# Optimization experiments

Measured on AMD Instinct MI355X. Metric: run time of the kernel, lower is better.

## Reference

```python
import jax, jax.numpy as jnp
import numpy as np

QMAX = 127.0  # symmetric int8
EPS = 1e-8

def _ste_round(v):
    # straight-through estimator round
    return v + jax.lax.stop_gradient(jnp.round(v) - v)

def fake_quant_act(x):
    # dynamic per-token symmetric 8-bit fake quant (last dim is features)
    scale = jnp.maximum(jnp.max(jnp.abs(x), axis=-1, keepdims=True) / QMAX, EPS)
    q = jnp.clip(_ste_round(x / scale), -QMAX, QMAX)
    return q * scale

def fake_quant_weight(w):
    # per-output-channel symmetric 8-bit fake quant; w: [out, in]
    scale = jnp.maximum(jnp.max(jnp.abs(w), axis=-1, keepdims=True) / QMAX, EPS)
    q = jnp.clip(_ste_round(w / scale), -QMAX, QMAX)
    return q * scale

def quant_linear(x, w):
    # fake-quant both operands, then dense matmul: [B,S,in] x [out,in] -> [B,S,out]
    return jnp.einsum('bsi,oi->bso', fake_quant_act(x), fake_quant_weight(w))

def setup_inputs() -> dict:
    key = jax.random.key(0)
    k1, k2, k3, k4 = jax.random.split(key, 4)
    B, S, H, I = 4, 2048, 2048, 6144
    return {
        'x': jax.random.normal(k1, (B, S, H), dtype=jnp.float32),
        'w_gate': jax.random.normal(k2, (I, H), dtype=jnp.float32) * 0.02,
        'w_up': jax.random.normal(k3, (I, H), dtype=jnp.float32) * 0.02,
        'w_down': jax.random.normal(k4, (H, I), dtype=jnp.float32) * 0.02,
    }

def reference(x, w_gate, w_up, w_down):
    gate = jax.nn.silu(quant_linear(x, w_gate))   # [B,S,I]
    up = quant_linear(x, w_up)                    # [B,S,I]
    return quant_linear(gate * up, w_down)        # [B,S,H]
```

## Files before the change

kernel.cpp:

```cpp
#include <hip/hip_runtime.h>
#include <hip/hip_bf16.h>
#include <math.h>

typedef __attribute__((ext_vector_type(4))) int intx4;

__device__ __forceinline__ void gload_lds16(const void* g, void* l) {
  __builtin_amdgcn_global_load_lds((__attribute__((address_space(1))) void*)g,
                                   (__attribute__((address_space(3))) void*)l,
                                   16, 0, 0);
}

__device__ __forceinline__ int pack4_i8(float a, float b, float c, float d) {
  return ((int)a & 255) | (((int)b & 255) << 8) | (((int)c & 255) << 16) | (((int)d & 255) << 24);
}

template<int NITER>
__global__ void quant_rows_i8_kernel(const float* __restrict__ src,
                                     signed char* __restrict__ dst,
                                     float* __restrict__ scales,
                                     int C) {
  const int row = blockIdx.x;
  const int t = threadIdx.x;
  const float4* s4 = (const float4*)(src + (size_t)row * C);
  float4 v[NITER];
  float amax = 0.0f;
#pragma unroll
  for (int i = 0; i < NITER; ++i) {
    v[i] = s4[t + (i << 8)];
    amax = fmaxf(amax, fmaxf(fmaxf(fabsf(v[i].x), fabsf(v[i].y)),
                             fmaxf(fabsf(v[i].z), fabsf(v[i].w))));
  }
#pragma unroll
  for (int off = 32; off > 0; off >>= 1)
    amax = fmaxf(amax, __shfl_xor(amax, off));
  __shared__ float red[4];
  if ((t & 63) == 0) red[t >> 6] = amax;
  __syncthreads();
  if (t == 0) {
    float m = fmaxf(fmaxf(red[0], red[1]), fmaxf(red[2], red[3]));
    float s = fmaxf(m * (1.0f / 127.0f), 1e-8f);
    red[0] = s;
    scales[row] = s;
  }
  __syncthreads();
  const float scale = red[0];
  int* o4 = (int*)(dst + (size_t)row * C);
#pragma unroll
  for (int i = 0; i < NITER; ++i) {
    const float q0 = fminf(fmaxf(rintf(v[i].x / scale), -127.0f), 127.0f);
    const float q1 = fminf(fmaxf(rintf(v[i].y / scale), -127.0f), 127.0f);
    const float q2 = fminf(fmaxf(rintf(v[i].z / scale), -127.0f), 127.0f);
    const float q3 = fminf(fmaxf(rintf(v[i].w / scale), -127.0f), 127.0f);
    o4[t + (i << 8)] = pack4_i8(q0, q1, q2, q3);
  }
}

template<bool DUAL>
__global__ __launch_bounds__(256, 2)
void gemm_i8_kernel(const signed char* __restrict__ A,
                    const signed char* __restrict__ B0,
                    const signed char* __restrict__ B1,
                    const float* __restrict__ sA,
                    const float* __restrict__ sB0,
                    const float* __restrict__ sB1,
                    float* __restrict__ out,
                    int N, int K) {
  extern __shared__ __align__(16) char smem[];
  char* const As  = smem;
  char* const Bs0 = smem + 16384;
  char* const Bs1 = smem + 32768;

  const int nTn = N >> 7;
  const int nwg = gridDim.x;
  const int bid = blockIdx.x;
  const int cpx = nwg >> 3;
  const int swz = (bid & 7) * cpx + (bid >> 3);
  const int tm = swz / nTn, tn = swz - tm * nTn;
  const int m0 = tm << 7, n0 = tn << 7;

  const int t = threadIdx.x;
  const int lane = t & 63;
  const int wid = t >> 6;
  const int wr = wid >> 1, wc = wid & 1;

  const intx4 zero = {0, 0, 0, 0};
  intx4 acc0[4][4];
  intx4 acc1[4][4];
#pragma unroll
  for (int i = 0; i < 4; ++i)
#pragma unroll
    for (int j = 0; j < 4; ++j) {
      acc0[i][j] = zero;
      if (DUAL) acc1[i][j] = zero;
    }

  for (int k0 = 0; k0 < K; k0 += 128) {
#pragma unroll
    for (int rr = 0; rr < 4; ++rr) {
      const int chunk = (rr << 8) + t;
      const int r = chunk >> 3;
      const int c8 = (chunk & 7) ^ (r & 7);
      gload_lds16(A + (size_t)(m0 + r) * K + (k0 + (c8 << 4)), As + (chunk << 4));
    }
#pragma unroll
    for (int rr = 0; rr < 4; ++rr) {
      const int chunk = (rr << 8) + t;
      const int r = chunk >> 3;
      const int c8 = (chunk & 7) ^ (r & 7);
      const size_t goff = (size_t)(n0 + r) * K + (k0 + (c8 << 4));
      gload_lds16(B0 + goff, Bs0 + (chunk << 4));
      if (DUAL) gload_lds16(B1 + goff, Bs1 + (chunk << 4));
    }
    __syncthreads();

#pragma unroll
    for (int ks = 0; ks < 2; ++ks) {
      intx4 af[4], bf0[4], bf1[4];
#pragma unroll
      for (int i = 0; i < 4; ++i) {
        const int r = (wr << 6) + (i << 4) + (lane & 15);
        const int c8 = (ks << 2) + (lane >> 4);
        af[i] = *(const intx4*)(As + r * 128 + ((c8 ^ (r & 7)) << 4));
      }
#pragma unroll
      for (int j = 0; j < 4; ++j) {
        const int r = (wc << 6) + (j << 4) + (lane & 15);
        const int c8 = (ks << 2) + (lane >> 4);
        const int off = r * 128 + ((c8 ^ (r & 7)) << 4);
        bf0[j] = *(const intx4*)(Bs0 + off);
        if (DUAL) bf1[j] = *(const intx4*)(Bs1 + off);
      }
#pragma unroll
      for (int i = 0; i < 4; ++i)
#pragma unroll
        for (int j = 0; j < 4; ++j) {
          acc0[i][j] = __builtin_amdgcn_mfma_i32_16x16x64_i8(af[i], bf0[j], acc0[i][j], 0, 0, 0);
          if (DUAL)
            acc1[i][j] = __builtin_amdgcn_mfma_i32_16x16x64_i8(af[i], bf1[j], acc1[i][j], 0, 0, 0);
        }
    }
    __syncthreads();
  }

  float sb0c[4], sb1c[4];
#pragma unroll
  for (int j = 0; j < 4; ++j) {
    const int col = n0 + (wc << 6) + (j << 4) + (lane & 15);
    sb0c[j] = sB0[col];
    if (DUAL) sb1c[j] = sB1[col];
  }
#pragma unroll
  for (int i = 0; i < 4; ++i) {
#pragma unroll
    for (int q = 0; q < 4; ++q) {
      const int row = m0 + (wr << 6) + (i << 4) + ((lane >> 4) << 2) + q;
      const float sa = sA[row];
      float* op = out + (size_t)row * N + n0 + (wc << 6) + (lane & 15);
#pragma unroll
      for (int j = 0; j < 4; ++j) {
        const float g = (float)acc0[i][j][q] * sa * sb0c[j];
        if (DUAL) {
          const float u = (float)acc1[i][j][q] * sa * sb1c[j];
          op[j << 4] = g / (1.0f + expf(-g)) * u;
        } else {
          op[j << 4] = g;
        }
      }
    }
  }
}

extern "C" void kernel_launch(void* const* d_in, const int* in_sizes, int n_in,
                              void* d_out, int out_size, void* d_ws, size_t ws_size,
                              hipStream_t stream) {
  const float* x  = (const float*)d_in[0];
  const float* wg = (const float*)d_in[1];
  const float* wu = (const float*)d_in[2];
  const float* wd = (const float*)d_in[3];
  float* out = (float*)d_out;

  const int M = 8192;
  const int H = 2048;
  const int I = 6144;

  char* ws = (char*)d_ws;
  signed char* xq  = (signed char*)(ws);
  signed char* wgq = (signed char*)(ws + 16777216);
  signed char* wuq = (signed char*)(ws + 29360128);
  signed char* wdq = (signed char*)(ws + 41943040);
  float* sx  = (float*)(ws + 54525952);
  float* swg = (float*)(ws + 54558720);
  float* swu = (float*)(ws + 54583296);
  float* swd = (float*)(ws + 54607872);
  float* sh  = (float*)(ws + 54616064);
  const size_t chunk_base = 54648832;

  size_t avail = (ws_size > chunk_base) ? (ws_size - chunk_base) : 0;
  long long c = (long long)(avail / ((size_t)I * 5));
  int CHUNK = (int)((c / 128) * 128);
  if (CHUNK > M) CHUNK = M;
  if (CHUNK < 128) CHUNK = 128;
  float* h = (float*)(ws + chunk_base);
  signed char* hq = (signed char*)(ws + chunk_base + (size_t)CHUNK * I * 4);

  quant_rows_i8_kernel<2><<<M, 256, 0, stream>>>(x,  xq,  sx,  H);
  quant_rows_i8_kernel<2><<<I, 256, 0, stream>>>(wg, wgq, swg, H);
  quant_rows_i8_kernel<2><<<I, 256, 0, stream>>>(wu, wuq, swu, H);
  quant_rows_i8_kernel<6><<<H, 256, 0, stream>>>(wd, wdq, swd, I);

  for (int m0 = 0; m0 < M; m0 += CHUNK) {
    const int Mc = (M - m0 < CHUNK) ? (M - m0) : CHUNK;
    gemm_i8_kernel<true><<<dim3((Mc / 128) * (I / 128)), 256, 49152, stream>>>(
        xq + (size_t)m0 * H, wgq, wuq, sx + m0, swg, swu, h, I, H);
    quant_rows_i8_kernel<6><<<Mc, 256, 0, stream>>>(h, hq, sh + m0, I);
    gemm_i8_kernel<false><<<dim3((Mc / 128) * (H / 128)), 256, 32768, stream>>>(
        hq, wdq, nullptr, sh + m0, swd, nullptr, out + (size_t)m0 * H, H, I);
  }
}
```

Measured before the change: 709.5 us.

## Replace int8 GEMM with 256x256 double-buffered pipelined kernel and split gate/up

Replaces the 128x128 single-buffered int8 GEMM with a 256x256 tile, 512-thread kernel. It uses 128KB of LDS, double-buffers the K slices and interleaves global-to-LDS prefetch with MFMA phases under s_setprio. The dual gate/up kernel is split into two launches. The first writes the gate result to h, and the second reads it back and applies SiLU times up. This adds an extra read and write of the large h buffer. Launch bounds of (512,2) with 128KB LDS per block may limit occupancy to one block per CU.

```diff
diff --git a/kernel.cpp b/kernel.cpp
--- a/kernel.cpp
+++ b/kernel.cpp
@@ -55,115 +55,149 @@
   }
 }
 
-template<bool DUAL>
-__global__ __launch_bounds__(256, 2)
-void gemm_i8_kernel(const signed char* __restrict__ A,
-                    const signed char* __restrict__ B0,
-                    const signed char* __restrict__ B1,
-                    const float* __restrict__ sA,
-                    const float* __restrict__ sB0,
-                    const float* __restrict__ sB1,
-                    float* __restrict__ out,
-                    int N, int K) {
+#define SBAR() __builtin_amdgcn_s_barrier()
+#define VMW(more) do { if (more) asm volatile("s_waitcnt vmcnt(4)" ::: "memory"); \
+                       else      asm volatile("s_waitcnt vmcnt(0)" ::: "memory"); } while (0)
+
+__device__ __forceinline__ void stage_plane(const signed char* __restrict__ mat,
+                                            int rowbase, int K, int kcol,
+                                            char* lds, int tid) {
+#pragma unroll
+  for (int u = 0; u < 2; ++u) {
+    const int c = (u << 9) + tid;
+    const int r = c >> 2;
+    const int src = (c & 3) ^ ((r >> 1) & 3);
+    gload_lds16(mat + (size_t)(rowbase + r) * K + (kcol + (src << 4)), lds + (c << 4));
+  }
+}
+
+template<int MODE>
+__global__ __launch_bounds__(512, 2)
+void gemm8p_kernel(const signed char* __restrict__ A,
+                   const signed char* __restrict__ B,
+                   const float* __restrict__ sA,
+                   const float* __restrict__ sB,
+                   float* __restrict__ out,
+                   int N, int K) {
   extern __shared__ __align__(16) char smem[];
-  char* const As  = smem;
-  char* const Bs0 = smem + 16384;
-  char* const Bs1 = smem + 32768;
-
-  const int nTn = N >> 7;
+  const int nTn = N >> 8;
   const int nwg = gridDim.x;
   const int bid = blockIdx.x;
   const int cpx = nwg >> 3;
   const int swz = (bid & 7) * cpx + (bid >> 3);
   const int tm = swz / nTn, tn = swz - tm * nTn;
-  const int m0 = tm << 7, n0 = tn << 7;
-
-  const int t = threadIdx.x;
-  const int lane = t & 63;
-  const int wid = t >> 6;
-  const int wr = wid >> 1, wc = wid & 1;
+  const int m0 = tm << 8, n0 = tn << 8;
+
+  const int tid = threadIdx.x;
+  const int lane = tid & 63;
+  const int wid = tid >> 6;
+  const int wr = wid >> 2, wc = wid & 3;
+  const int l15 = lane & 15, slq = lane >> 4;
+  const int NT = K >> 7;
 
   const intx4 zero = {0, 0, 0, 0};
-  intx4 acc0[4][4];
-  intx4 acc1[4][4];
-#pragma unroll
-  for (int i = 0; i < 4; ++i)
-#pragma unroll
-    for (int j = 0; j < 4; ++j) {
-      acc0[i][j] = zero;
-      if (DUAL) acc1[i][j] = zero;
-    }
-
-  for (int k0 = 0; k0 < K; k0 += 128) {
-#pragma unroll
-    for (int rr = 0; rr < 4; ++rr) {
-      const int chunk = (rr << 8) + t;
-      const int r = chunk >> 3;
-      const int c8 = (chunk & 7) ^ (r & 7);
-      gload_lds16(A + (size_t)(m0 + r) * K + (k0 + (c8 << 4)), As + (chunk << 4));
-    }
-#pragma unroll
-    for (int rr = 0; rr < 4; ++rr) {
-      const int chunk = (rr << 8) + t;
-      const int r = chunk >> 3;
-      const int c8 = (chunk & 7) ^ (r & 7);
-      const size_t goff = (size_t)(n0 + r) * K + (k0 + (c8 << 4));
-      gload_lds16(B0 + goff, Bs0 + (chunk << 4));
-      if (DUAL) gload_lds16(B1 + goff, Bs1 + (chunk << 4));
-    }
-    __syncthreads();
-
-#pragma unroll
-    for (int ks = 0; ks < 2; ++ks) {
-      intx4 af[4], bf0[4], bf1[4];
-#pragma unroll
-      for (int i = 0; i < 4; ++i) {
-        const int r = (wr << 6) + (i << 4) + (lane & 15);
-        const int c8 = (ks << 2) + (lane >> 4);
-        af[i] = *(const intx4*)(As + r * 128 + ((c8 ^ (r & 7)) << 4));
-      }
+  intx4 acc[8][4];
+#pragma unroll
+  for (int i = 0; i < 8; ++i)
+#pragma unroll
+    for (int j = 0; j < 4; ++j) acc[i][j] = zero;
+
+  auto rdA = [&](char* buf, int ks, int i) -> intx4 {
+    const int r = (wr << 7) + (i << 4) + l15;
+    return *(const intx4*)(buf + (ks << 14) + (r << 6) + ((slq ^ ((r >> 1) & 3)) << 4));
+  };
+  auto rdB = [&](char* buf, int ks, int j) -> intx4 {
+    const int r = (wc << 6) + (j << 4) + l15;
+    return *(const intx4*)(buf + 32768 + (ks << 14) + (r << 6) + ((slq ^ ((r >> 1) & 3)) << 4));
+  };
+
+  stage_plane(A, m0, K, 0,  smem,          tid);
+  stage_plane(B, n0, K, 0,  smem + 32768,  tid);
+  stage_plane(A, m0, K, 64, smem + 16384,  tid);
+  stage_plane(B, n0, K, 64, smem + 49152,  tid);
+  asm volatile("s_waitcnt vmcnt(0)" ::: "memory");
+  SBAR();
+
+  for (int t = 0; t < NT; ++t) {
+    char* const bufc = smem + ((t & 1) << 16);
+    char* const bufn = smem + (((t & 1) ^ 1) << 16);
+    const int kn = (t + 1) << 7;
+    const bool more = (t + 1) < NT;
+    intx4 a[8], b[4];
+
+#pragma unroll
+    for (int i = 0; i < 8; ++i) a[i] = rdA(bufc, 0, i);
+    b[0] = rdB(bufc, 0, 0); b[1] = rdB(bufc, 0, 1);
+    if (more) stage_plane(A, m0, K, kn, bufn, tid);
+    SBAR();
+    __builtin_amdgcn_s_setprio(1);
+#pragma unroll
+    for (int i = 0; i < 8; ++i) {
+      acc[i][0] = __builtin_amdgcn_mfma_i32_16x16x64_i8(a[i], b[0], acc[i][0], 0, 0, 0);
+      acc[i][1] = __builtin_amdgcn_mfma_i32_16x16x64_i8(a[i], b[1], acc[i][1], 0, 0, 0);
+    }
+    __builtin_amdgcn_s_setprio(0);
+    SBAR();
+
+    b[2] = rdB(bufc, 0, 2); b[3] = rdB(bufc, 0, 3);
+    if (more) stage_plane(B, n0, K, kn, bufn + 32768, tid);
+    SBAR();
+    __builtin_amdgcn_s_setprio(1);
+#pragma unroll
+    for (int i = 0; i < 8; ++i) {
+      acc[i][2] = __builtin_amdgcn_mfma_i32_16x16x64_i8(a[i], b[2], acc[i][2], 0, 0, 0);
+      acc[i][3] = __builtin_amdgcn_mfma_i32_16x16x64_i8(a[i], b[3], acc[i][3], 0, 0, 0);
+    }
+    __builtin_amdgcn_s_setprio(0);
+    VMW(more);
+    SBAR();
+
+#pragma unroll
+    for (int i = 0; i < 8; ++i) a[i] = rdA(bufc, 1, i);
+    b[0] = rdB(bufc, 1, 0); b[1] = rdB(bufc, 1, 1);
+    if (more) stage_plane(A, m0, K, kn + 64, bufn + 16384, tid);
+    SBAR();
+    __builtin_amdgcn_s_setprio(1);
+#pragma unroll
+    for (int i = 0; i < 8; ++i) {
+      acc[i][0] = __builtin_amdgcn_mfma_i32_16x16x64_i8(a[i], b[0], acc[i][0], 0, 0, 0);
+      acc[i][1] = __builtin_amdgcn_mfma_i32_16x16x64_i8(a[i], b[1], acc[i][1], 0, 0, 0);
+    }
+    __builtin_amdgcn_s_setprio(0);
+    SBAR();
+
+    b[2] = rdB(bufc, 1, 2); b[3] = rdB(bufc, 1, 3);
+    if (more) stage_plane(B, n0, K, kn + 64, bufn + 49152, tid);
+    SBAR();
+    __builtin_amdgcn_s_setprio(1);
+#pragma unroll
+    for (int i = 0; i < 8; ++i) {
+      acc[i][2] = __builtin_amdgcn_mfma_i32_16x16x64_i8(a[i], b[2], acc[i][2], 0, 0, 0);
+      acc[i][3] = __builtin_amdgcn_mfma_i32_16x16x64_i8(a[i], b[3], acc[i][3], 0, 0, 0);
+    }
+    __builtin_amdgcn_s_setprio(0);
+    VMW(more);
+    SBAR();
+  }
+
+  float sbc[4];
+#pragma unroll
+  for (int j = 0; j < 4; ++j) sbc[j] = sB[n0 + (wc << 6) + (j << 4) + l15];
+#pragma unroll
+  for (int i = 0; i < 8; ++i) {
+#pragma unroll
+    for (int q = 0; q < 4; ++q) {
+      const int row = m0 + (wr << 7) + (i << 4) + (slq << 2) + q;
+      const float sa = sA[row];
+      float* op = out + (size_t)row * N + n0 + (wc << 6) + l15;
 #pragma unroll
       for (int j = 0; j < 4; ++j) {
-        const int r = (wc << 6) + (j << 4) + (lane & 15);
-        const int c8 = (ks << 2) + (lane >> 4);
-        const int off = r * 128 + ((c8 ^ (r & 7)) << 4);
-        bf0[j] = *(const intx4*)(Bs0 + off);
-        if (DUAL) bf1[j] = *(const intx4*)(Bs1 + off);
-      }
-#pragma unroll
-      for (int i = 0; i < 4; ++i)
-#pragma unroll
-        for (int j = 0; j < 4; ++j) {
-          acc0[i][j] = __builtin_amdgcn_mfma_i32_16x16x64_i8(af[i], bf0[j], acc0[i][j], 0, 0, 0);
-          if (DUAL)
-            acc1[i][j] = __builtin_amdgcn_mfma_i32_16x16x64_i8(af[i], bf1[j], acc1[i][j], 0, 0, 0);
-        }
-    }
-    __syncthreads();
-  }
-
-  float sb0c[4], sb1c[4];
-#pragma unroll
-  for (int j = 0; j < 4; ++j) {
-    const int col = n0 + (wc << 6) + (j << 4) + (lane & 15);
-    sb0c[j] = sB0[col];
-    if (DUAL) sb1c[j] = sB1[col];
-  }
-#pragma unroll
-  for (int i = 0; i < 4; ++i) {
-#pragma unroll
-    for (int q = 0; q < 4; ++q) {
-      const int row = m0 + (wr << 6) + (i << 4) + ((lane >> 4) << 2) + q;
-      const float sa = sA[row];
-      float* op = out + (size_t)row * N + n0 + (wc << 6) + (lane & 15);
-#pragma unroll
-      for (int j = 0; j < 4; ++j) {
-        const float g = (float)acc0[i][j][q] * sa * sb0c[j];
-        if (DUAL) {
-          const float u = (float)acc1[i][j][q] * sa * sb1c[j];
-          op[j << 4] = g / (1.0f + expf(-g)) * u;
+        const float v = (float)acc[i][j][q] * sa * sbc[j];
+        if (MODE == 1) {
+          const float g = op[j << 4];
+          op[j << 4] = g / (1.0f + expf(-g)) * v;
         } else {
-          op[j << 4] = g;
+          op[j << 4] = v;
         }
       }
     }
@@ -179,9 +213,12 @@
   const float* wd = (const float*)d_in[3];
   float* out = (float*)d_out;
 
-  const int M = 8192;
-  const int H = 2048;
-  const int I = 6144;
+  const int M = 8192, H = 2048, I = 6144;
+
+  hipFuncSetAttribute((const void*)gemm8p_kernel<0>,
+                      hipFuncAttributeMaxDynamicSharedMemorySize, 131072);
+  hipFuncSetAttribute((const void*)gemm8p_kernel<1>,
+                      hipFuncAttributeMaxDynamicSharedMemorySize, 131072);
 
   char* ws = (char*)d_ws;
   signed char* xq  = (signed char*)(ws);
@@ -197,9 +234,9 @@
 
   size_t avail = (ws_size > chunk_base) ? (ws_size - chunk_base) : 0;
   long long c = (long long)(avail / ((size_t)I * 5));
-  int CHUNK = (int)((c / 128) * 128);
+  int CHUNK = (int)((c / 256) * 256);
   if (CHUNK > M) CHUNK = M;
-  if (CHUNK < 128) CHUNK = 128;
+  if (CHUNK < 256) CHUNK = 256;
   float* h = (float*)(ws + chunk_base);
   signed char* hq = (signed char*)(ws + chunk_base + (size_t)CHUNK * I * 4);
 
@@ -210,10 +247,13 @@
 
   for (int m0 = 0; m0 < M; m0 += CHUNK) {
     const int Mc = (M - m0 < CHUNK) ? (M - m0) : CHUNK;
-    gemm_i8_kernel<true><<<dim3((Mc / 128) * (I / 128)), 256, 49152, stream>>>(
-        xq + (size_t)m0 * H, wgq, wuq, sx + m0, swg, swu, h, I, H);
+    const int gTiles = Mc / 256;
+    gemm8p_kernel<0><<<dim3(gTiles * (I / 256)), 512, 131072, stream>>>(
+        xq + (size_t)m0 * H, wgq, sx + m0, swg, h, I, H);
+    gemm8p_kernel<1><<<dim3(gTiles * (I / 256)), 512, 131072, stream>>>(
+        xq + (size_t)m0 * H, wuq, sx + m0, swu, h, I, H);
     quant_rows_i8_kernel<6><<<Mc, 256, 0, stream>>>(h, hq, sh + m0, I);
-    gemm_i8_kernel<false><<<dim3((Mc / 128) * (H / 128)), 256, 32768, stream>>>(
-        hq, wdq, nullptr, sh + m0, swd, nullptr, out + (size_t)m0 * H, H, I);
-  }
-}
+    gemm8p_kernel<0><<<dim3(gTiles * (H / 256)), 512, 131072, stream>>>(
+        hq, wdq, sh + m0, swd, out + (size_t)m0 * H, H, I);
+  }
+}
```

New measurement: 791.7 us. 11.6% more time.
